# Kernel tuning notes

Measured on AMD Instinct MI355X. Metric: run time of the kernel, lower is better.

## Reference

```python
import jax, jax.numpy as jnp
import numpy as np

N_NODES = 50000
N_EDGES = 800000
IN_DIM = 256
OUT_DIM = 128
ALPHA = 0.2  # leaky_relu negative slope


def setup_inputs() -> dict:
    key = jax.random.key(0)
    k1, k2, k3, k4, k5 = jax.random.split(key, 5)
    h = jax.random.normal(k1, (N_NODES, IN_DIM), dtype=jnp.float32)
    src = jax.random.randint(k2, (N_EDGES,), 0, N_NODES)
    dst = jax.random.randint(k3, (N_EDGES,), 0, N_NODES)
    W_fc = jax.random.normal(k4, (IN_DIM, OUT_DIM), dtype=jnp.float32) * (1.0 / np.sqrt(IN_DIM))
    attn_w = jax.random.normal(k5, (2 * OUT_DIM,), dtype=jnp.float32) * (1.0 / np.sqrt(2 * OUT_DIM))
    return {"h": h, "src": src, "dst": dst, "W_fc": W_fc, "attn_w": attn_w}


def reference(h, src, dst, W_fc, attn_w):
    n = h.shape[0]
    # fc projection: z = h @ W  -> [N, out]
    z = h @ W_fc
    # edge attention logit: attn_fc(cat(z_src, z_dst)) = z_src@a1 + z_dst@a2
    a1 = attn_w[:OUT_DIM]
    a2 = attn_w[OUT_DIM:]
    logit = z[src] @ a1 + z[dst] @ a2               # [E]
    e = jnp.where(logit >= 0, logit, ALPHA * logit)  # leaky_relu
    # segment softmax over incoming edges of each destination node
    m = jax.ops.segment_max(e, dst, num_segments=n)   # [N], -inf if no edges
    m = jnp.where(jnp.isfinite(m), m, 0.0)
    ex = jnp.exp(e - m[dst])                          # [E]
    denom = jax.ops.segment_sum(ex, dst, num_segments=n)  # [N]
    denom = jnp.where(denom > 0, denom, 1.0)
    alpha_e = ex / denom[dst]                         # [E]
    # weighted scatter-sum of source features
    h_out = jax.ops.segment_sum(alpha_e[:, None] * z[src], dst, num_segments=n)  # [N, out]
    # concat=True -> elu activation
    return jnp.where(h_out > 0, h_out, jnp.expm1(h_out))
```

## Files before the change

### kernel.cpp

```cpp
#include <hip/hip_runtime.h>
#include <math.h>

#define N_NODES 50000
#define N_EDGES 800000
#define IN_DIM 256
#define OUT_DIM 128
#define ALPHA 0.2f

#define BKT 196
#define EPB 4096
#define HIST_NB 196
#define GEMM_NB 391

typedef __attribute__((ext_vector_type(8))) short short8;
typedef __attribute__((ext_vector_type(4))) float f32x4;
typedef __attribute__((ext_vector_type(2))) float f32x2;

#define OFF_ZB    0u
#define OFF_S1    12800000u
#define OFF_S2    13000000u
#define OFF_OFFS2 13200000u
#define OFF_WT    13400064u
#define OFF_HIST  13465600u
#define OFF_BBASE 13619264u
#define OFF_BTOT  13772928u
#define OFF_TMP   13773712u
#define OFF_SRCS  16973712u

static __device__ __forceinline__ unsigned short f2bf_rne(float f) {
    unsigned int u = __float_as_uint(f);
    unsigned int r = (u + 0x7FFFu + ((u >> 16) & 1u)) >> 16;
    return (unsigned short)r;
}
static __device__ __forceinline__ unsigned int pack2bf(float lo, float hi) {
    return (unsigned int)f2bf_rne(lo) | ((unsigned int)f2bf_rne(hi) << 16);
}

__global__ __launch_bounds__(256) void wt_k(const float* __restrict__ W,
                                            unsigned short* __restrict__ WT) {
    int idx = (blockIdx.x * 256 + threadIdx.x) * 8;
    int c = idx >> 8, k0 = idx & 255;
    unsigned int uu[4];
#pragma unroll
    for (int q = 0; q < 4; q++) {
        float lo = W[(size_t)(k0 + 2 * q) * OUT_DIM + c];
        float hi = W[(size_t)(k0 + 2 * q + 1) * OUT_DIM + c];
        uu[q] = pack2bf(lo, hi);
    }
    *(uint4*)(WT + idx) = make_uint4(uu[0], uu[1], uu[2], uu[3]);
}

__global__ __launch_bounds__(512) void gemm_hist(const float* __restrict__ h,
                                                 const unsigned short* __restrict__ WT,
                                                 const float* __restrict__ attn,
                                                 unsigned short* __restrict__ zb,
                                                 float* __restrict__ s1,
                                                 float* __restrict__ s2,
                                                 const int* __restrict__ dst,
                                                 int* __restrict__ hist) {
    __shared__ char smem[32768];
    const int t = threadIdx.x;

    if (blockIdx.x >= GEMM_NB) {
        int hb = blockIdx.x - GEMM_NB;
        int* hcnt = (int*)smem;
        for (int i = t; i < BKT; i += 512) hcnt[i] = 0;
        __syncthreads();
#pragma unroll
        for (int q = 0; q < 8; q++) {
            int e = hb * EPB + q * 512 + t;
            if (e < N_EDGES) atomicAdd(&hcnt[dst[e] >> 8], 1);
        }
        __syncthreads();
        for (int i = t; i < BKT; i += 512) hist[hb * BKT + i] = hcnt[i];
        return;
    }

    const int lane = t & 63, w = t >> 6;
    const int row0 = blockIdx.x * 128;
    const int m16 = lane & 15, kb = lane >> 4;

    const int rA = row0 + w * 16 + m16;
    const float* hrow = h + (size_t)min(rA, N_NODES - 1) * IN_DIM + kb * 8;

    f32x4 acc[8];
#pragma unroll
    for (int ct = 0; ct < 8; ct++) acc[ct] = (f32x4){0.f, 0.f, 0.f, 0.f};

    float4 v0 = *(const float4*)(hrow);
    float4 v1 = *(const float4*)(hrow + 4);

#pragma unroll
    for (int half = 0; half < 2; half++) {
        if (half) __syncthreads();
#pragma unroll
        for (int q = 0; q < 4; q++) {
            int G = t * 4 + q;
            int cc = G >> 4, gs = G & 15;
            const uint4 v = *(const uint4*)(WT + (size_t)cc * IN_DIM + half * 128 + gs * 8);
            *(uint4*)(smem + cc * 256 + ((gs ^ (cc & 7)) * 16)) = v;
        }
        __syncthreads();
#pragma unroll
        for (int kcl = 0; kcl < 4; kcl++) {
            const float4 c0 = v0, c1 = v1;
            int nk = half * 4 + kcl + 1;
            if (nk < 8) {
                v0 = *(const float4*)(hrow + nk * 32);
                v1 = *(const float4*)(hrow + nk * 32 + 4);
            }
            short8 af;
            af[0] = (short)f2bf_rne(c0.x); af[1] = (short)f2bf_rne(c0.y);
            af[2] = (short)f2bf_rne(c0.z); af[3] = (short)f2bf_rne(c0.w);
            af[4] = (short)f2bf_rne(c1.x); af[5] = (short)f2bf_rne(c1.y);
            af[6] = (short)f2bf_rne(c1.z); af[7] = (short)f2bf_rne(c1.w);
            const char* bbase = smem + m16 * 256 + (((kcl * 4 + kb) ^ (m16 & 7)) * 16);
#pragma unroll
            for (int ct = 0; ct < 8; ct++) {
                const short8 bf = *(const short8*)(bbase + ct * 4096);
                acc[ct] = __builtin_amdgcn_mfma_f32_16x16x32_bf16(af, bf, acc[ct], 0, 0, 0);
            }
        }
    }

    float a1v[8], a2v[8];
#pragma unroll
    for (int ct = 0; ct < 8; ct++) {
        a1v[ct] = attn[ct * 16 + m16];
        a2v[ct] = attn[OUT_DIM + ct * 16 + m16];
    }
#pragma unroll
    for (int i = 0; i < 4; i++) {
        int rr = row0 + w * 16 + kb * 4 + i;
        float q1 = 0.f, q2 = 0.f;
#pragma unroll
        for (int ct = 0; ct < 8; ct++) {
            q1 += acc[ct][i] * a1v[ct];
            q2 += acc[ct][i] * a2v[ct];
        }
        q1 += __shfl_xor(q1, 1); q1 += __shfl_xor(q1, 2);
        q1 += __shfl_xor(q1, 4); q1 += __shfl_xor(q1, 8);
        q2 += __shfl_xor(q2, 1); q2 += __shfl_xor(q2, 2);
        q2 += __shfl_xor(q2, 4); q2 += __shfl_xor(q2, 8);
        if (m16 == 0 && rr < N_NODES) { s1[rr] = q1; s2[rr] = q2; }
        if (rr < N_NODES) {
#pragma unroll
            for (int ct = 0; ct < 8; ct++)
                zb[(size_t)rr * OUT_DIM + ct * 16 + m16] = f2bf_rne(acc[ct][i]);
        }
    }
}

__global__ __launch_bounds__(256) void colscan(const int* __restrict__ hist,
                                               int* __restrict__ bbase,
                                               int* __restrict__ btot) {
    __shared__ int s[256];
    int t = threadIdx.x, b = blockIdx.x;
    int d0 = (t < BKT) ? hist[t * BKT + b] : 0;
    s[t] = d0;
    __syncthreads();
    int v = d0;
    for (int ofs = 1; ofs < 256; ofs <<= 1) {
        int add = (t >= ofs) ? s[t - ofs] : 0;
        __syncthreads();
        v += add;
        s[t] = v;
        __syncthreads();
    }
    if (t < BKT) bbase[t * BKT + b] = v - d0;
    if (t == BKT - 1) btot[b] = v;
}

__global__ __launch_bounds__(512) void scatter_b(const int* __restrict__ src,
                                                 const int* __restrict__ dst,
                                                 const int* __restrict__ bbase,
                                                 const int* __restrict__ btot,
                                                 unsigned int* __restrict__ tmp) {
    __shared__ int s[256];
    __shared__ int bb[BKT];
    __shared__ int bstartL[BKT];
    __shared__ int cur[BKT];
    int t = threadIdx.x, m = blockIdx.x;

    for (int i = t; i < BKT; i += 512) { bb[i] = bbase[m * BKT + i]; cur[i] = 0; }
    int d0 = 0;
    if (t < 256) { d0 = (t < BKT) ? btot[t] : 0; s[t] = d0; }
    __syncthreads();
    int v = d0;
    for (int ofs = 1; ofs < 256; ofs <<= 1) {
        int add = (t < 256 && t >= ofs) ? s[t - ofs] : 0;
        __syncthreads();
        if (t < 256) { v += add; s[t] = v; }
        __syncthreads();
    }
    if (t < BKT) bstartL[t] = v - d0;
    __syncthreads();

#pragma unroll
    for (int q = 0; q < 8; q++) {
        int e = m * EPB + q * 512 + t;
        if (e < N_EDGES) {
            int d = dst[e];
            int bkt = d >> 8;
            int r = atomicAdd(&cur[bkt], 1);
            tmp[bstartL[bkt] + bb[bkt] + r] =
                ((unsigned int)d << 16) | (unsigned int)src[e];
        }
    }
}

__global__ __launch_bounds__(512) void bucket_sort(const unsigned int* __restrict__ tmp,
                                                   const int* __restrict__ btot,
                                                   unsigned short* __restrict__ srcs,
                                                   int* __restrict__ offs2) {
    __shared__ int s[256];
    __shared__ int cnt[256];
    __shared__ int cur[256];
    int t = threadIdx.x, b = blockIdx.x;

    int d0 = 0;
    if (t < 256) { d0 = (t < BKT) ? btot[t] : 0; s[t] = d0; cnt[t] = 0; }
    __syncthreads();
    int v = d0;
    for (int ofs = 1; ofs < 256; ofs <<= 1) {
        int add = (t < 256 && t >= ofs) ? s[t - ofs] : 0;
        __syncthreads();
        if (t < 256) { v += add; s[t] = v; }
        __syncthreads();
    }
    __syncthreads();
    const int myCount = btot[b];
    const int myStart = s[b] - myCount;

    for (int i = t; i < myCount; i += 512)
        atomicAdd(&cnt[(tmp[myStart + i] >> 16) & 255], 1);
    __syncthreads();

    int c0 = 0;
    if (t < 256) { c0 = cnt[t]; s[t] = c0; }
    __syncthreads();
    int cv = c0;
    for (int ofs = 1; ofs < 256; ofs <<= 1) {
        int add = (t < 256 && t >= ofs) ? s[t - ofs] : 0;
        __syncthreads();
        if (t < 256) { cv += add; s[t] = cv; }
        __syncthreads();
    }
    if (t < 256) {
        int excl = cv - c0;
        int node = b * 256 + t;
        if (node < N_NODES) offs2[node] = myStart + excl;
        cur[t] = excl;
    }
    if (b == 0 && t == 0) offs2[N_NODES] = N_EDGES;
    __syncthreads();

    for (int i = t; i < myCount; i += 512) {
        unsigned int u = tmp[myStart + i];
        int r = atomicAdd(&cur[(u >> 16) & 255], 1);
        srcs[myStart + r] = (unsigned short)(u & 0xFFFFu);
    }
}

__global__ __launch_bounds__(256) void aggregate(const unsigned short* __restrict__ zb,
                                                 const int* __restrict__ offs2,
                                                 const unsigned short* __restrict__ srcs,
                                                 const float* __restrict__ s1,
                                                 const float* __restrict__ s2,
                                                 float* __restrict__ out) {
    int wid = (blockIdx.x * blockDim.x + threadIdx.x) >> 6;
    int lane = threadIdx.x & 63;
    if (wid >= N_NODES) return;
    const int g = lane >> 3;
    const int l = lane & 7;
    float* outp = out + (size_t)wid * OUT_DIM + l * 16 + g * 2;

    int base = offs2[wid];
    int len = offs2[wid + 1] - base;
    if (len == 0) {
        *(float2*)outp = make_float2(0.f, 0.f);
        return;
    }
    const float s2v = s2[wid];

    float sum = 0.f;
    f32x2 acc2[8];
#pragma unroll
    for (int k = 0; k < 8; k++) acc2[k] = (f32x2){0.f, 0.f};

    for (int c0 = 0; c0 < len; c0 += 64) {
        int i = c0 + lane;
        float ex = 0.f;
        int sj = 0;
        if (i < len) {
            sj = srcs[base + i];
            float lg = s1[sj] + s2v;
            lg = (lg >= 0.f) ? lg : ALPHA * lg;
            ex = __expf(lg);
        }
        sum += ex;
        int cnt = min(64, len - c0);
        int j0 = 0;
        for (; j0 + 16 <= cnt; j0 += 16) {
            int ja = j0 + g, jb = j0 + 8 + g;
            float wa = __shfl(ex, ja), wb = __shfl(ex, jb);
            int sa = __shfl(sj, ja), sb = __shfl(sj, jb);
            const uint4* rpa = (const uint4*)(zb + (size_t)sa * OUT_DIM);
            const uint4* rpb = (const uint4*)(zb + (size_t)sb * OUT_DIM);
            const uint4 a0 = rpa[l * 2];
            const uint4 a1 = rpa[l * 2 + 1];
            const uint4 b0 = rpb[l * 2];
            const uint4 b1 = rpb[l * 2 + 1];
#pragma unroll
            for (int k = 0; k < 4; k++) {
                unsigned int u = (&a0.x)[k];
                f32x2 f;
                f.x = __uint_as_float(u << 16);
                f.y = __uint_as_float(u & 0xFFFF0000u);
                acc2[k] += wa * f;
                u = (&b0.x)[k];
                f.x = __uint_as_float(u << 16);
                f.y = __uint_as_float(u & 0xFFFF0000u);
                acc2[k] += wb * f;
            }
#pragma unroll
            for (int k = 0; k < 4; k++) {
                unsigned int u = (&a1.x)[k];
                f32x2 f;
                f.x = __uint_as_float(u << 16);
                f.y = __uint_as_float(u & 0xFFFF0000u);
                acc2[4 + k] += wa * f;
                u = (&b1.x)[k];
                f.x = __uint_as_float(u << 16);
                f.y = __uint_as_float(u & 0xFFFF0000u);
                acc2[4 + k] += wb * f;
            }
        }
        for (; j0 < cnt; j0 += 8) {
            int j = j0 + g;
            float wj = __shfl(ex, j);
            int s = __shfl(sj, j);
            if (j < cnt) {
                const uint4* rp = (const uint4*)(zb + (size_t)s * OUT_DIM);
                const uint4 v0 = rp[l * 2];
                const uint4 v1 = rp[l * 2 + 1];
#pragma unroll
                for (int k = 0; k < 4; k++) {
                    unsigned int u = (&v0.x)[k];
                    f32x2 f;
                    f.x = __uint_as_float(u << 16);
                    f.y = __uint_as_float(u & 0xFFFF0000u);
                    acc2[k] += wj * f;
                }
#pragma unroll
                for (int k = 0; k < 4; k++) {
                    unsigned int u = (&v1.x)[k];
                    f32x2 f;
                    f.x = __uint_as_float(u << 16);
                    f.y = __uint_as_float(u & 0xFFFF0000u);
                    acc2[4 + k] += wj * f;
                }
            }
        }
    }
#pragma unroll
    for (int k = 0; k < 8; k++) {
        acc2[k].x += __shfl_xor(acc2[k].x, 8);
        acc2[k].y += __shfl_xor(acc2[k].y, 8);
        acc2[k].x += __shfl_xor(acc2[k].x, 16);
        acc2[k].y += __shfl_xor(acc2[k].y, 16);
        acc2[k].x += __shfl_xor(acc2[k].x, 32);
        acc2[k].y += __shfl_xor(acc2[k].y, 32);
    }
#pragma unroll
    for (int m = 32; m >= 1; m >>= 1) sum += __shfl_xor(sum, m);
    float inv = (sum > 0.f) ? 1.f / sum : 1.f;

    float a0 = acc2[g].x * inv;
    float a1 = acc2[g].y * inv;
    float2 o;
    o.x = (a0 > 0.f) ? a0 : expm1f(a0);
    o.y = (a1 > 0.f) ? a1 : expm1f(a1);
    *(float2*)outp = o;
}

extern "C" void kernel_launch(void* const* d_in, const int* in_sizes, int n_in,
                              void* d_out, int out_size, void* d_ws, size_t ws_size,
                              hipStream_t stream) {
    const float* h      = (const float*)d_in[0];
    const int*   src    = (const int*)d_in[1];
    const int*   dst    = (const int*)d_in[2];
    const float* W_fc   = (const float*)d_in[3];
    const float* attn_w = (const float*)d_in[4];
    float* out = (float*)d_out;

    char* ws = (char*)d_ws;
    unsigned short* zb = (unsigned short*)(ws + OFF_ZB);
    float* s1       = (float*)(ws + OFF_S1);
    float* s2       = (float*)(ws + OFF_S2);
    int*   offs2    = (int*)(ws + OFF_OFFS2);
    unsigned short* WT = (unsigned short*)(ws + OFF_WT);
    int*   hist     = (int*)(ws + OFF_HIST);
    int*   bbase    = (int*)(ws + OFF_BBASE);
    int*   btot     = (int*)(ws + OFF_BTOT);
    unsigned int* tmp = (unsigned int*)(ws + OFF_TMP);
    unsigned short* srcs = (unsigned short*)(ws + OFF_SRCS);

    wt_k<<<16, 256, 0, stream>>>(W_fc, WT);
    gemm_hist<<<GEMM_NB + HIST_NB, 512, 0, stream>>>(h, WT, attn_w, zb, s1, s2, dst, hist);
    colscan<<<BKT, 256, 0, stream>>>(hist, bbase, btot);
    scatter_b<<<HIST_NB, 512, 0, stream>>>(src, dst, bbase, btot, tmp);
    bucket_sort<<<BKT, 512, 0, stream>>>(tmp, btot, srcs, offs2);
    aggregate<<<(N_NODES * 64) / 256, 256, 0, stream>>>(zb, offs2, srcs, s1, s2, out);
}
```

Measured before the change: 83.63 us.

## Drop colscan kernel and remap aggregate to one edge per wave-step

The histogram is now written transposed, and scatter_b and bucket_sort each recompute bucket totals and per-block prefix bases by serially summing rows of it. This removes the separate colscan launch and its intermediate buffers, at the cost of redundant per-block work of about 196 loads per thread. The aggregate kernel changes from processing 8 edges in parallel (8 lanes per row, uint4 loads, then a cross-lane reduction) to processing edges one at a time. Each lane loads 4 bytes of the source row, with the index and weight broadcast via readlane, so the final shuffle reduction disappears but there are many more small dependent loads.

```diff
diff --git a/kernel.cpp b/kernel.cpp
--- a/kernel.cpp
+++ b/kernel.cpp
@@ -14,7 +14,6 @@
 
 typedef __attribute__((ext_vector_type(8))) short short8;
 typedef __attribute__((ext_vector_type(4))) float f32x4;
-typedef __attribute__((ext_vector_type(2))) float f32x2;
 
 #define OFF_ZB    0u
 #define OFF_S1    12800000u
@@ -22,10 +21,8 @@
 #define OFF_OFFS2 13200000u
 #define OFF_WT    13400064u
 #define OFF_HIST  13465600u
-#define OFF_BBASE 13619264u
-#define OFF_BTOT  13772928u
-#define OFF_TMP   13773712u
-#define OFF_SRCS  16973712u
+#define OFF_TMP   13619264u
+#define OFF_SRCS  16819264u
 
 static __device__ __forceinline__ unsigned short f2bf_rne(float f) {
     unsigned int u = __float_as_uint(f);
@@ -57,7 +54,7 @@
                                                  float* __restrict__ s1,
                                                  float* __restrict__ s2,
                                                  const int* __restrict__ dst,
-                                                 int* __restrict__ hist) {
+                                                 int* __restrict__ histT) {
     __shared__ char smem[32768];
     const int t = threadIdx.x;
 
@@ -72,7 +69,7 @@
             if (e < N_EDGES) atomicAdd(&hcnt[dst[e] >> 8], 1);
         }
         __syncthreads();
-        for (int i = t; i < BKT; i += 512) hist[hb * BKT + i] = hcnt[i];
+        for (int i = t; i < BKT; i += 512) histT[i * HIST_NB + hb] = hcnt[i];
         return;
     }
 
@@ -151,46 +148,35 @@
     }
 }
 
-__global__ __launch_bounds__(256) void colscan(const int* __restrict__ hist,
-                                               int* __restrict__ bbase,
-                                               int* __restrict__ btot) {
-    __shared__ int s[256];
-    int t = threadIdx.x, b = blockIdx.x;
-    int d0 = (t < BKT) ? hist[t * BKT + b] : 0;
-    s[t] = d0;
-    __syncthreads();
-    int v = d0;
-    for (int ofs = 1; ofs < 256; ofs <<= 1) {
-        int add = (t >= ofs) ? s[t - ofs] : 0;
-        __syncthreads();
-        v += add;
-        s[t] = v;
-        __syncthreads();
-    }
-    if (t < BKT) bbase[t * BKT + b] = v - d0;
-    if (t == BKT - 1) btot[b] = v;
-}
-
 __global__ __launch_bounds__(512) void scatter_b(const int* __restrict__ src,
                                                  const int* __restrict__ dst,
-                                                 const int* __restrict__ bbase,
-                                                 const int* __restrict__ btot,
+                                                 const int* __restrict__ histT,
                                                  unsigned int* __restrict__ tmp) {
-    __shared__ int s[256];
-    __shared__ int bb[BKT];
+    __shared__ int sS[256];
+    __shared__ int bbL[BKT];
     __shared__ int bstartL[BKT];
     __shared__ int cur[BKT];
     int t = threadIdx.x, m = blockIdx.x;
 
-    for (int i = t; i < BKT; i += 512) { bb[i] = bbase[m * BKT + i]; cur[i] = 0; }
-    int d0 = 0;
-    if (t < 256) { d0 = (t < BKT) ? btot[t] : 0; s[t] = d0; }
+    int tot = 0, bb = 0;
+    if (t < BKT) {
+        const int* row = histT + t * HIST_NB;
+        for (int m2 = 0; m2 < BKT; m2++) {
+            int v = row[m2];
+            tot += v;
+            bb += (m2 < m) ? v : 0;
+        }
+        bbL[t] = bb;
+        cur[t] = 0;
+    }
+    int d0 = (t < BKT) ? tot : 0;
+    if (t < 256) sS[t] = d0;
     __syncthreads();
     int v = d0;
     for (int ofs = 1; ofs < 256; ofs <<= 1) {
-        int add = (t < 256 && t >= ofs) ? s[t - ofs] : 0;
-        __syncthreads();
-        if (t < 256) { v += add; s[t] = v; }
+        int add = (t < 256 && t >= ofs) ? sS[t - ofs] : 0;
+        __syncthreads();
+        if (t < 256) { v += add; sS[t] = v; }
         __syncthreads();
     }
     if (t < BKT) bstartL[t] = v - d0;
@@ -203,47 +189,53 @@
             int d = dst[e];
             int bkt = d >> 8;
             int r = atomicAdd(&cur[bkt], 1);
-            tmp[bstartL[bkt] + bb[bkt] + r] =
+            tmp[bstartL[bkt] + bbL[bkt] + r] =
                 ((unsigned int)d << 16) | (unsigned int)src[e];
         }
     }
 }
 
 __global__ __launch_bounds__(512) void bucket_sort(const unsigned int* __restrict__ tmp,
-                                                   const int* __restrict__ btot,
+                                                   const int* __restrict__ histT,
                                                    unsigned short* __restrict__ srcs,
                                                    int* __restrict__ offs2) {
-    __shared__ int s[256];
+    __shared__ int sS[256];
     __shared__ int cnt[256];
     __shared__ int cur[256];
+    __shared__ int msS, mcS;
     int t = threadIdx.x, b = blockIdx.x;
 
-    int d0 = 0;
-    if (t < 256) { d0 = (t < BKT) ? btot[t] : 0; s[t] = d0; cnt[t] = 0; }
+    int tot = 0;
+    if (t < BKT) {
+        const int* row = histT + t * HIST_NB;
+        for (int m2 = 0; m2 < BKT; m2++) tot += row[m2];
+    }
+    int d0 = (t < BKT) ? tot : 0;
+    if (t < 256) { sS[t] = d0; cnt[t] = 0; }
     __syncthreads();
     int v = d0;
     for (int ofs = 1; ofs < 256; ofs <<= 1) {
-        int add = (t < 256 && t >= ofs) ? s[t - ofs] : 0;
-        __syncthreads();
-        if (t < 256) { v += add; s[t] = v; }
-        __syncthreads();
-    }
-    __syncthreads();
-    const int myCount = btot[b];
-    const int myStart = s[b] - myCount;
+        int add = (t < 256 && t >= ofs) ? sS[t - ofs] : 0;
+        __syncthreads();
+        if (t < 256) { v += add; sS[t] = v; }
+        __syncthreads();
+    }
+    if (t == b) { msS = v - d0; mcS = d0; }
+    __syncthreads();
+    const int myStart = msS, myCount = mcS;
 
     for (int i = t; i < myCount; i += 512)
         atomicAdd(&cnt[(tmp[myStart + i] >> 16) & 255], 1);
     __syncthreads();
 
     int c0 = 0;
-    if (t < 256) { c0 = cnt[t]; s[t] = c0; }
+    if (t < 256) { c0 = cnt[t]; sS[t] = c0; }
     __syncthreads();
     int cv = c0;
     for (int ofs = 1; ofs < 256; ofs <<= 1) {
-        int add = (t < 256 && t >= ofs) ? s[t - ofs] : 0;
-        __syncthreads();
-        if (t < 256) { cv += add; s[t] = cv; }
+        int add = (t < 256 && t >= ofs) ? sS[t - ofs] : 0;
+        __syncthreads();
+        if (t < 256) { cv += add; sS[t] = cv; }
         __syncthreads();
     }
     if (t < 256) {
@@ -271,22 +263,19 @@
     int wid = (blockIdx.x * blockDim.x + threadIdx.x) >> 6;
     int lane = threadIdx.x & 63;
     if (wid >= N_NODES) return;
-    const int g = lane >> 3;
-    const int l = lane & 7;
-    float* outp = out + (size_t)wid * OUT_DIM + l * 16 + g * 2;
+    float2* outp = (float2*)(out + (size_t)wid * OUT_DIM) + lane;
 
     int base = offs2[wid];
     int len = offs2[wid + 1] - base;
     if (len == 0) {
-        *(float2*)outp = make_float2(0.f, 0.f);
+        *outp = make_float2(0.f, 0.f);
         return;
     }
     const float s2v = s2[wid];
+    const unsigned int voff = lane * 2;
 
     float sum = 0.f;
-    f32x2 acc2[8];
-#pragma unroll
-    for (int k = 0; k < 8; k++) acc2[k] = (f32x2){0.f, 0.f};
+    float ax = 0.f, ay = 0.f;
 
     for (int c0 = 0; c0 < len; c0 += 64) {
         int i = c0 + lane;
@@ -300,88 +289,34 @@
         }
         sum += ex;
         int cnt = min(64, len - c0);
-        int j0 = 0;
-        for (; j0 + 16 <= cnt; j0 += 16) {
-            int ja = j0 + g, jb = j0 + 8 + g;
-            float wa = __shfl(ex, ja), wb = __shfl(ex, jb);
-            int sa = __shfl(sj, ja), sb = __shfl(sj, jb);
-            const uint4* rpa = (const uint4*)(zb + (size_t)sa * OUT_DIM);
-            const uint4* rpb = (const uint4*)(zb + (size_t)sb * OUT_DIM);
-            const uint4 a0 = rpa[l * 2];
-            const uint4 a1 = rpa[l * 2 + 1];
-            const uint4 b0 = rpb[l * 2];
-            const uint4 b1 = rpb[l * 2 + 1];
-#pragma unroll
-            for (int k = 0; k < 4; k++) {
-                unsigned int u = (&a0.x)[k];
-                f32x2 f;
-                f.x = __uint_as_float(u << 16);
-                f.y = __uint_as_float(u & 0xFFFF0000u);
-                acc2[k] += wa * f;
-                u = (&b0.x)[k];
-                f.x = __uint_as_float(u << 16);
-                f.y = __uint_as_float(u & 0xFFFF0000u);
-                acc2[k] += wb * f;
+        int j = 0;
+        for (; j + 4 <= cnt; j += 4) {
+#pragma unroll
+            for (int q = 0; q < 4; q++) {
+                int s = __builtin_amdgcn_readlane(sj, j + q);
+                float wj = __int_as_float(__builtin_amdgcn_readlane(__float_as_int(ex), j + q));
+                unsigned int u = *(const unsigned int*)(zb + (size_t)(unsigned)s * OUT_DIM + voff);
+                ax += wj * __uint_as_float(u << 16);
+                ay += wj * __uint_as_float(u & 0xFFFF0000u);
             }
-#pragma unroll
-            for (int k = 0; k < 4; k++) {
-                unsigned int u = (&a1.x)[k];
-                f32x2 f;
-                f.x = __uint_as_float(u << 16);
-                f.y = __uint_as_float(u & 0xFFFF0000u);
-                acc2[4 + k] += wa * f;
-                u = (&b1.x)[k];
-                f.x = __uint_as_float(u << 16);
-                f.y = __uint_as_float(u & 0xFFFF0000u);
-                acc2[4 + k] += wb * f;
-            }
-        }
-        for (; j0 < cnt; j0 += 8) {
-            int j = j0 + g;
-            float wj = __shfl(ex, j);
-            int s = __shfl(sj, j);
-            if (j < cnt) {
-                const uint4* rp = (const uint4*)(zb + (size_t)s * OUT_DIM);
-                const uint4 v0 = rp[l * 2];
-                const uint4 v1 = rp[l * 2 + 1];
-#pragma unroll
-                for (int k = 0; k < 4; k++) {
-                    unsigned int u = (&v0.x)[k];
-                    f32x2 f;
-                    f.x = __uint_as_float(u << 16);
-                    f.y = __uint_as_float(u & 0xFFFF0000u);
-                    acc2[k] += wj * f;
-                }
-#pragma unroll
-                for (int k = 0; k < 4; k++) {
-                    unsigned int u = (&v1.x)[k];
-                    f32x2 f;
-                    f.x = __uint_as_float(u << 16);
-                    f.y = __uint_as_float(u & 0xFFFF0000u);
-                    acc2[4 + k] += wj * f;
-                }
-            }
-        }
-    }
-#pragma unroll
-    for (int k = 0; k < 8; k++) {
-        acc2[k].x += __shfl_xor(acc2[k].x, 8);
-        acc2[k].y += __shfl_xor(acc2[k].y, 8);
-        acc2[k].x += __shfl_xor(acc2[k].x, 16);
-        acc2[k].y += __shfl_xor(acc2[k].y, 16);
-        acc2[k].x += __shfl_xor(acc2[k].x, 32);
-        acc2[k].y += __shfl_xor(acc2[k].y, 32);
+        }
+        for (; j < cnt; j++) {
+            int s = __builtin_amdgcn_readlane(sj, j);
+            float wj = __int_as_float(__builtin_amdgcn_readlane(__float_as_int(ex), j));
+            unsigned int u = *(const unsigned int*)(zb + (size_t)(unsigned)s * OUT_DIM + voff);
+            ax += wj * __uint_as_float(u << 16);
+            ay += wj * __uint_as_float(u & 0xFFFF0000u);
+        }
     }
 #pragma unroll
     for (int m = 32; m >= 1; m >>= 1) sum += __shfl_xor(sum, m);
     float inv = (sum > 0.f) ? 1.f / sum : 1.f;
 
-    float a0 = acc2[g].x * inv;
-    float a1 = acc2[g].y * inv;
+    float a0 = ax * inv, a1 = ay * inv;
     float2 o;
     o.x = (a0 > 0.f) ? a0 : expm1f(a0);
     o.y = (a1 > 0.f) ? a1 : expm1f(a1);
-    *(float2*)outp = o;
+    *outp = o;
 }
 
 extern "C" void kernel_launch(void* const* d_in, const int* in_sizes, int n_in,
@@ -400,16 +335,13 @@
     float* s2       = (float*)(ws + OFF_S2);
     int*   offs2    = (int*)(ws + OFF_OFFS2);
     unsigned short* WT = (unsigned short*)(ws + OFF_WT);
-    int*   hist     = (int*)(ws + OFF_HIST);
-    int*   bbase    = (int*)(ws + OFF_BBASE);
-    int*   btot     = (int*)(ws + OFF_BTOT);
+    int*   histT    = (int*)(ws + OFF_HIST);
     unsigned int* tmp = (unsigned int*)(ws + OFF_TMP);
     unsigned short* srcs = (unsigned short*)(ws + OFF_SRCS);
 
     wt_k<<<16, 256, 0, stream>>>(W_fc, WT);
-    gemm_hist<<<GEMM_NB + HIST_NB, 512, 0, stream>>>(h, WT, attn_w, zb, s1, s2, dst, hist);
-    colscan<<<BKT, 256, 0, stream>>>(hist, bbase, btot);
-    scatter_b<<<HIST_NB, 512, 0, stream>>>(src, dst, bbase, btot, tmp);
-    bucket_sort<<<BKT, 512, 0, stream>>>(tmp, btot, srcs, offs2);
+    gemm_hist<<<GEMM_NB + HIST_NB, 512, 0, stream>>>(h, WT, attn_w, zb, s1, s2, dst, histT);
+    scatter_b<<<HIST_NB, 512, 0, stream>>>(src, dst, histT, tmp);
+    bucket_sort<<<BKT, 512, 0, stream>>>(tmp, histT, srcs, offs2);
     aggregate<<<(N_NODES * 64) / 256, 256, 0, stream>>>(zb, offs2, srcs, s1, s2, out);
 }
```

Result: slower. 86.12 us (+3.0%).
